# Kernel optimization log

Hardware: AMD Instinct MI355X
Metric: run time of the kernel (lower is better)

The kernel has to match this reference:

```python
import jax, jax.numpy as jnp
import numpy as np

B, S, C, H = 64, 512, 256, 128
P = S  # predict_length defaults to seq_length


def _linear_init(k, fan_in, fan_out):
    bound = 1.0 / np.sqrt(fan_in)
    kw, kb = jax.random.split(k)
    w = jax.random.uniform(kw, (fan_in, fan_out), minval=-bound, maxval=bound, dtype=jnp.float32)
    b = jax.random.uniform(kb, (fan_out,), minval=-bound, maxval=bound, dtype=jnp.float32)
    return w, b


def setup_inputs() -> dict:
    key = jax.random.key(0)
    ks = jax.random.split(key, 10)
    x = jax.random.normal(ks[0], (B, S, C), dtype=jnp.float32)
    wq1, bq1 = _linear_init(ks[1], S, H)
    wk1, bk1 = _linear_init(ks[2], S, H)
    wq2, bq2 = _linear_init(ks[3], S // 2, H)
    wk2, bk2 = _linear_init(ks[4], S // 2, H)
    wq3, bq3 = _linear_init(ks[5], S // 4, H)
    wk3, bk3 = _linear_init(ks[6], S // 4, H)
    wv, bv = _linear_init(ks[7], S, S)
    wo, bo = _linear_init(ks[8], S, P)
    return dict(x=x, wq1=wq1, bq1=bq1, wk1=wk1, bk1=bk1,
                wq2=wq2, bq2=bq2, wk2=wk2, bk2=bk2,
                wq3=wq3, bq3=bq3, wk3=wk3, bk3=bk3,
                wv=wv, bv=bv, wo=wo, bo=bo)


def _channel_attn(xl, wq, bq, wk, bk):
    # xl: [b', C, L]; q,k: [b', C, H]; returns softmax channel-attention [b', C, C]
    q = xl @ wq + bq
    k = xl @ wk + bk
    scores = jnp.einsum('bch,bdh->bcd', q, k) / jnp.sqrt(jnp.asarray(H, q.dtype))
    return jax.nn.softmax(scores, axis=-1)


def reference(x, wq1, bq1, wk1, bk1, wq2, bq2, wk2, bk2, wq3, bq3, wk3, bk3, wv, bv, wo, bo):
    b, s, c = x.shape
    x1 = jnp.swapaxes(x, -2, -1)                                   # [B, C, S]
    x2 = jnp.swapaxes(x.reshape(b * 2, s // 2, c), -2, -1)          # [2B, C, S/2]
    x3 = jnp.swapaxes(x.reshape(b * 4, s // 4, c), -2, -1)          # [4B, C, S/4]
    a1 = _channel_attn(x1, wq1, bq1, wk1, bk1)                      # [B, C, C]
    a2 = _channel_attn(x2, wq2, bq2, wk2, bk2).reshape(b, 2, c, c).mean(axis=1)
    a3 = _channel_attn(x3, wq3, bq3, wk3, bk3).reshape(b, 4, c, c).mean(axis=1)
    stacked = jnp.stack([a1, a2, a3], axis=0)                       # [3, B, C, C]
    gate = jax.nn.softmax(stacked, axis=0)                          # softmax over scales
    attn = (stacked * gate).sum(axis=0)                             # gated multi-scale combine [B, C, C]
    v = x1 @ wv + bv                                                # [B, C, S]
    out = (attn @ v) @ wo + bo                                      # [B, C, P]
    return jnp.swapaxes(out, -2, -1)                                # [B, P, C]
```

## Files before the change

### kernel.cpp

```cpp
#include <hip/hip_runtime.h>
#include <hip/hip_bf16.h>


typedef __attribute__((ext_vector_type(8))) short bf16x8;
typedef __attribute__((ext_vector_type(4))) float f32x4;
typedef __attribute__((ext_vector_type(8))) unsigned short ushort8;

typedef __attribute__((address_space(1))) void* as1vp;
typedef __attribute__((address_space(3))) void* as3vp;

__device__ __forceinline__ void gl2lds16(const void* g, void* l) {
  __builtin_amdgcn_global_load_lds((as1vp)(void*)g, (as3vp)l, 16, 0, 0);
}

__device__ __forceinline__ float bf2f(unsigned short u) {
  union { unsigned int i; float f; } v; v.i = ((unsigned int)u) << 16; return v.f;
}
__device__ __forceinline__ unsigned short f2bf(float f) {
  union { float f; unsigned int i; } v; v.f = f;
  unsigned int r = v.i + 0x7FFFu + ((v.i >> 16) & 1u);
  return (unsigned short)(r >> 16);
}
__device__ __forceinline__ unsigned long long pack4bf(float a, float b, float c, float d) {
  return (unsigned long long)f2bf(a) | ((unsigned long long)f2bf(b) << 16) |
         ((unsigned long long)f2bf(c) << 32) | ((unsigned long long)f2bf(d) << 48);
}

__global__ void __launch_bounds__(256) tcast_all(
    const float* __restrict__ x,
    const float* __restrict__ wq1, const float* __restrict__ wk1,
    const float* __restrict__ wq2, const float* __restrict__ wk2,
    const float* __restrict__ wq3, const float* __restrict__ wk3,
    const float* __restrict__ wv, const float* __restrict__ wo,
    unsigned short* __restrict__ XT,
    unsigned short* __restrict__ W1, unsigned short* __restrict__ W2,
    unsigned short* __restrict__ W3, unsigned short* __restrict__ WVNT,
    unsigned short* __restrict__ WOT) {
  const int bid = blockIdx.x;
  const int t = threadIdx.x;
  if (bid >= 2168) {
    long i0 = (long)(bid - 2168) * 2048 + t * 8;
    f32x4 a = *(const f32x4*)(wv + i0);
    f32x4 b = *(const f32x4*)(wv + i0 + 4);
    ushort8 o;
#pragma unroll
    for (int j = 0; j < 4; ++j) { o[j] = f2bf(a[j]); o[4 + j] = f2bf(b[j]); }
    *(ushort8*)(WVNT + i0) = o;
    return;
  }
  __shared__ float lds[64][68];
  const float* S; unsigned short* D; int R, Cc, r0, c0, rowoff = 0;
  if (bid < 2048) {
    int bz = bid >> 5, i = bid & 31;
    S = x + (long)bz * 131072; D = XT + (long)bz * 131072;
    R = 512; Cc = 256; r0 = (i & 7) * 64; c0 = (i >> 3) * 64;
  } else {
    int wb = bid - 2048;
    if (wb < 32) {
      int m = wb >> 4, i = wb & 15;
      S = m ? wk1 : wq1; D = W1; R = 512; Cc = 128;
      r0 = (i & 7) * 64; c0 = (i >> 3) * 64; rowoff = m * 128;
    } else if (wb < 48) {
      int m = (wb - 32) >> 3, i = (wb - 32) & 7;
      S = m ? wk2 : wq2; D = W2; R = 256; Cc = 128;
      r0 = (i & 3) * 64; c0 = (i >> 2) * 64; rowoff = m * 128;
    } else if (wb < 56) {
      int m = (wb - 48) >> 2, i = (wb - 48) & 3;
      S = m ? wk3 : wq3; D = W3; R = 128; Cc = 128;
      r0 = (i & 1) * 64; c0 = (i >> 1) * 64; rowoff = m * 128;
    } else {
      int i = wb - 56; S = wo; D = WOT; R = 512; Cc = 512;
      r0 = (i & 7) * 64; c0 = (i >> 3) * 64;
    }
  }
  {
    const int row = t >> 2, cq = (t & 3) * 16;
    const float* Sp = S + (long)(r0 + row) * Cc + c0 + cq;
#pragma unroll
    for (int j = 0; j < 4; ++j)
      *(f32x4*)&lds[row][cq + j * 4] = *(const f32x4*)(Sp + j * 4);
  }
  __syncthreads();
  {
    const int rq = (t & 15) * 4, ccb = t >> 4;
#pragma unroll
    for (int j = 0; j < 4; ++j) {
      int cc = ccb + j * 16;
      *(unsigned long long*)(D + (long)(c0 + cc + rowoff) * R + r0 + rq) =
          pack4bf(lds[rq][cc], lds[rq + 1][cc], lds[rq + 2][cc], lds[rq + 3][cc]);
    }
  }
}

__global__ void __launch_bounds__(512) proj_all8(
    const unsigned short* __restrict__ XT,
    const unsigned short* __restrict__ W1, const unsigned short* __restrict__ W2,
    const unsigned short* __restrict__ W3,
    const unsigned short* __restrict__ WOT, const unsigned short* __restrict__ WVNT,
    unsigned short* __restrict__ WVOT, float* __restrict__ BVO,
    const float* __restrict__ bv,
    unsigned short* __restrict__ Q1, unsigned short* __restrict__ Q2,
    unsigned short* __restrict__ Q3,
    const float* __restrict__ bq1, const float* __restrict__ bk1,
    const float* __restrict__ bq2, const float* __restrict__ bk2,
    const float* __restrict__ bq3, const float* __restrict__ bk3) {
  extern __shared__ char smem[];
  const int z = blockIdx.z;
  const int t = threadIdx.x, lane = t & 63, wid = t >> 6;

  if (z >= 464) {
    int p0 = (z - 464) * 128 + wid * 16;
    f32x4 b0 = *(const f32x4*)(bv + lane * 8);
    f32x4 b1 = *(const f32x4*)(bv + lane * 8 + 4);
#pragma unroll
    for (int i = 0; i < 16; ++i) {
      int p = p0 + i;
      bf16x8 wrow = *(const bf16x8*)(WOT + (long)p * 512 + lane * 8);
      float s = 0.0f;
#pragma unroll
      for (int j = 0; j < 4; ++j) {
        s += b0[j] * bf2f((unsigned short)wrow[j]);
        s += b1[j] * bf2f((unsigned short)wrow[4 + j]);
      }
#pragma unroll
      for (int off = 1; off < 64; off <<= 1) s += __shfl_xor(s, off, 64);
      if (lane == 0) BVO[p] = s;
    }
    return;
  }

  const int srow = t >> 3, ssl = t & 7;

  if (z >= 448) {
    const int w = z - 448;
    const int m0 = (w >> 2) * 128, n0 = (w & 3) * 128;
    const unsigned short* Ab = WOT + (long)m0 * 512;
    const unsigned short* Bb = WVNT + (long)n0 * 512;
    const int wmb = (wid >> 2) * 64, wnb = (wid & 3) * 32;
    f32x4 acc[4][2] = {};
    auto stageS = [&](int buf, int k0) {
      char* s = smem + buf * 32768;
#pragma unroll
      for (int i = 0; i < 2; ++i) {
        int row = i * 64 + srow;
        gl2lds16(Ab + (long)row * 512 + k0 + (ssl ^ (row & 7)) * 8, s + i * 8192 + t * 16);
        gl2lds16(Bb + (long)row * 512 + k0 + (ssl ^ (row & 7)) * 8, s + 16384 + i * 8192 + t * 16);
      }
    };
    stageS(0, 0);
    stageS(1, 64);
    for (int j = 0; j < 8; ++j) {
      if (j < 7) asm volatile("s_waitcnt vmcnt(4)" ::: "memory");
      else       asm volatile("s_waitcnt vmcnt(0)" ::: "memory");
      __builtin_amdgcn_s_barrier();
      if (j + 2 < 8) stageS((j + 2) % 3, (j + 2) * 64);
      const char* s = smem + (j % 3) * 32768;
#pragma unroll
      for (int kk = 0; kk < 2; ++kk) {
        const int slot = kk * 4 + (lane >> 4);
        bf16x8 af[4], bfr[2];
#pragma unroll
        for (int mi = 0; mi < 4; ++mi) {
          int row = wmb + mi * 16 + (lane & 15);
          af[mi] = *(const bf16x8*)(s + row * 128 + 16 * (slot ^ (row & 7)));
        }
#pragma unroll
        for (int ni = 0; ni < 2; ++ni) {
          int row = wnb + ni * 16 + (lane & 15);
          bfr[ni] = *(const bf16x8*)(s + 16384 + row * 128 + 16 * (slot ^ (row & 7)));
        }
#pragma unroll
        for (int mi = 0; mi < 4; ++mi)
#pragma unroll
          for (int ni = 0; ni < 2; ++ni)
            acc[mi][ni] = __builtin_amdgcn_mfma_f32_16x16x32_bf16(af[mi], bfr[ni], acc[mi][ni], 0, 0, 0);
      }
    }
#pragma unroll
    for (int ni = 0; ni < 2; ++ni) {
      int col = n0 + wnb + ni * 16 + (lane & 15);
#pragma unroll
      for (int mi = 0; mi < 4; ++mi) {
        int rowb = m0 + wmb + mi * 16 + (lane >> 4) * 4;
#pragma unroll
        for (int r = 0; r < 4; ++r)
          WVOT[(long)(rowb + r) * 512 + col] = f2bf(acc[mi][ni][r]);
      }
    }
    return;
  }

  const unsigned short* Ab; const unsigned short* Bw; unsigned short* O;
  const float *bq, *bk; int K;
  if (z < 64) {
    K = 512; Bw = W1; O = Q1 + (long)z * 65536; bq = bq1; bk = bk1;
    Ab = XT + (long)z * 131072;
  } else if (z < 192) {
    int u = z - 64; K = 256; Bw = W2; O = Q2 + (long)u * 65536; bq = bq2; bk = bk2;
    Ab = XT + (long)(u >> 1) * 131072 + (u & 1) * 256;
  } else {
    int u = z - 192; K = 128; Bw = W3; O = Q3 + (long)u * 65536; bq = bq3; bk = bk3;
    Ab = XT + (long)(u >> 2) * 131072 + (u & 3) * 128;
  }
  const int wmb = (wid >> 1) * 64, wnb = (wid & 1) * 128;

  auto stage = [&](int buf, int k0) {
    char* s = smem + buf * 65536;
#pragma unroll
    for (int i = 0; i < 4; ++i) {
      int row = i * 64 + srow;
      int sc = (ssl ^ (row & 7)) * 8;
      gl2lds16(Ab + (long)row * 512 + k0 + sc, s + i * 8192 + t * 16);
      gl2lds16(Bw + (long)row * K + k0 + sc, s + 32768 + i * 8192 + t * 16);
    }
  };

  f32x4 acc[4][8] = {};
  const int nst = K >> 6;
  stage(0, 0);
  __syncthreads();
  int cur = 0;
  for (int j = 0; j < nst; ++j) {
    if (j + 1 < nst) stage(cur ^ 1, (j + 1) * 64);
    const char* s = smem + cur * 65536;
#pragma unroll
    for (int kk = 0; kk < 2; ++kk) {
      const int slot = kk * 4 + (lane >> 4);
      bf16x8 af[4], bfr[8];
#pragma unroll
      for (int mi = 0; mi < 4; ++mi) {
        int row = wmb + mi * 16 + (lane & 15);
        af[mi] = *(const bf16x8*)(s + row * 128 + 16 * (slot ^ (row & 7)));
      }
#pragma unroll
      for (int ni = 0; ni < 8; ++ni) {
        int row = wnb + ni * 16 + (lane & 15);
        bfr[ni] = *(const bf16x8*)(s + 32768 + row * 128 + 16 * (slot ^ (row & 7)));
      }
#pragma unroll
      for (int mi = 0; mi < 4; ++mi)
#pragma unroll
        for (int ni = 0; ni < 8; ++ni)
          acc[mi][ni] = __builtin_amdgcn_mfma_f32_16x16x32_bf16(af[mi], bfr[ni], acc[mi][ni], 0, 0, 0);
    }
    __syncthreads();
    cur ^= 1;
  }
#pragma unroll
  for (int ni = 0; ni < 8; ++ni) {
    int colL = wnb + ni * 16 + (lane & 15);
    float bv_ = (colL < 128) ? bq[colL] : bk[colL - 128];
#pragma unroll
    for (int mi = 0; mi < 4; ++mi) {
      int rowb = wmb + mi * 16 + (lane >> 4) * 4;
#pragma unroll
      for (int r = 0; r < 4; ++r)
        O[(long)(rowb + r) * 256 + colL] = f2bf(acc[mi][ni][r] + bv_);
    }
  }
}

__global__ void __launch_bounds__(256) scores_mean(
    const unsigned short* __restrict__ QK2, const unsigned short* __restrict__ QK3,
    unsigned short* __restrict__ A2P, unsigned short* __restrict__ A3P) {
  __shared__ unsigned short Qs[64 * 64];
  __shared__ unsigned short Ks[256 * 64];
  const int bid = blockIdx.x;
  const unsigned short* QK; unsigned short* Aout; int NS, b, m0idx;
  if (bid < 256) { NS = 4; b = bid >> 2; m0idx = bid & 3; QK = QK3; Aout = A3P; }
  else { int u = bid - 256; NS = 2; b = u >> 2; m0idx = u & 3; QK = QK2; Aout = A2P; }
  const int m0 = m0idx * 64;
  const int t = threadIdx.x, lane = t & 63, w = t >> 6;
  const int r8 = t >> 3, sl = t & 7;
  const float sc = 0.088388347648318447f;
  const float invNS = 1.0f / NS;
  f32x4 avg[16] = {};
  for (int h = 0; h < NS; ++h) {
    const unsigned short* base = QK + ((long)(b * NS + h) << 16);
    f32x4 acc[16] = {};
    for (int kc = 0; kc < 2; ++kc) {
#pragma unroll
      for (int i = 0; i < 2; ++i) {
        int row = i * 32 + r8;
        gl2lds16(base + (long)(m0 + row) * 256 + kc * 64 + (sl ^ (row & 7)) * 8,
                 (char*)Qs + i * 4096 + t * 16);
      }
#pragma unroll
      for (int i = 0; i < 8; ++i) {
        int row = i * 32 + r8;
        gl2lds16(base + (long)row * 256 + 128 + kc * 64 + (sl ^ (row & 7)) * 8,
                 (char*)Ks + i * 4096 + t * 16);
      }
      __syncthreads();
#pragma unroll
      for (int kk = 0; kk < 2; ++kk) {
        const int qrow = w * 16 + (lane & 15);
        const int slot = kk * 4 + (lane >> 4);
        bf16x8 qf = *(const bf16x8*)((char*)Qs + qrow * 128 + 16 * (slot ^ (qrow & 7)));
#pragma unroll
        for (int ni = 0; ni < 16; ++ni) {
          int krow = ni * 16 + (lane & 15);
          bf16x8 kf = *(const bf16x8*)((char*)Ks + krow * 128 + 16 * (slot ^ (krow & 7)));
          acc[ni] = __builtin_amdgcn_mfma_f32_16x16x32_bf16(qf, kf, acc[ni], 0, 0, 0);
        }
      }
      __syncthreads();
    }
#pragma unroll
    for (int r = 0; r < 4; ++r) {
      float mx = -1e30f;
#pragma unroll
      for (int ni = 0; ni < 16; ++ni) mx = fmaxf(mx, acc[ni][r]);
#pragma unroll
      for (int off = 1; off < 16; off <<= 1) mx = fmaxf(mx, __shfl_xor(mx, off, 64));
      float s = 0.0f;
#pragma unroll
      for (int ni = 0; ni < 16; ++ni) {
        float p = __expf((acc[ni][r] - mx) * sc);
        acc[ni][r] = p;
        s += p;
      }
#pragma unroll
      for (int off = 1; off < 16; off <<= 1) s += __shfl_xor(s, off, 64);
      float f = invNS / s;
#pragma unroll
      for (int ni = 0; ni < 16; ++ni) avg[ni][r] += acc[ni][r] * f;
    }
  }
  unsigned short* Of = Aout + (((long)b * 4 + m0idx) * 256 + t) * 64;
#pragma unroll
  for (int r = 0; r < 4; ++r) {
    ushort8 lo, hi;
#pragma unroll
    for (int j = 0; j < 8; ++j) { lo[j] = f2bf(avg[j][r]); hi[j] = f2bf(avg[8 + j][r]); }
    *(ushort8*)(Of + r * 16) = lo;
    *(ushort8*)(Of + r * 16 + 8) = hi;
  }
}

__global__ void __launch_bounds__(256) scores1_gate(
    const unsigned short* __restrict__ QK1, const unsigned short* __restrict__ A2P,
    const unsigned short* __restrict__ A3P, unsigned short* __restrict__ ATTN) {
  __shared__ unsigned short Qs[64 * 64];
  __shared__ unsigned short Ks[256 * 64];
  const int bid = blockIdx.x;
  const int b = bid >> 2, m0 = (bid & 3) * 64;
  const unsigned short* base = QK1 + ((long)b << 16);
  const int t = threadIdx.x, lane = t & 63, w = t >> 6;
  const int r8 = t >> 3, sl = t & 7;
  f32x4 acc[16] = {};
  for (int kc = 0; kc < 2; ++kc) {
#pragma unroll
    for (int i = 0; i < 2; ++i) {
      int row = i * 32 + r8;
      gl2lds16(base + (long)(m0 + row) * 256 + kc * 64 + (sl ^ (row & 7)) * 8,
               (char*)Qs + i * 4096 + t * 16);
    }
#pragma unroll
    for (int i = 0; i < 8; ++i) {
      int row = i * 32 + r8;
      gl2lds16(base + (long)row * 256 + 128 + kc * 64 + (sl ^ (row & 7)) * 8,
               (char*)Ks + i * 4096 + t * 16);
    }
    __syncthreads();
#pragma unroll
    for (int kk = 0; kk < 2; ++kk) {
      const int qrow = w * 16 + (lane & 15);
      const int slot = kk * 4 + (lane >> 4);
      bf16x8 qf = *(const bf16x8*)((char*)Qs + qrow * 128 + 16 * (slot ^ (qrow & 7)));
#pragma unroll
      for (int ni = 0; ni < 16; ++ni) {
        int krow = ni * 16 + (lane & 15);
        bf16x8 kf = *(const bf16x8*)((char*)Ks + krow * 128 + 16 * (slot ^ (krow & 7)));
        acc[ni] = __builtin_amdgcn_mfma_f32_16x16x32_bf16(qf, kf, acc[ni], 0, 0, 0);
      }
    }
    __syncthreads();
  }
  const float sc = 0.088388347648318447f;
#pragma unroll
  for (int r = 0; r < 4; ++r) {
    float mx = -1e30f;
#pragma unroll
    for (int ni = 0; ni < 16; ++ni) mx = fmaxf(mx, acc[ni][r]);
#pragma unroll
    for (int off = 1; off < 16; off <<= 1) mx = fmaxf(mx, __shfl_xor(mx, off, 64));
    float s = 0.0f;
#pragma unroll
    for (int ni = 0; ni < 16; ++ni) {
      float p = __expf((acc[ni][r] - mx) * sc);
      acc[ni][r] = p;
      s += p;
    }
#pragma unroll
    for (int off = 1; off < 16; off <<= 1) s += __shfl_xor(s, off, 64);
    float inv = 1.0f / s;
    long fidx = ((long)bid * 256 + t) * 64 + r * 16;
    ushort8 a2l = *(const ushort8*)(A2P + fidx);
    ushort8 a2h = *(const ushort8*)(A2P + fidx + 8);
    ushort8 a3l = *(const ushort8*)(A3P + fidx);
    ushort8 a3h = *(const ushort8*)(A3P + fidx + 8);
    int row = m0 + w * 16 + (lane >> 4) * 4 + r;
    long roff = ((long)b << 16) + (long)row * 256 + (lane & 15);
#pragma unroll
    for (int j = 0; j < 8; ++j) {
      float A1 = acc[j][r] * inv;
      float A2 = bf2f(a2l[j]), A3 = bf2f(a3l[j]);
      float m = fmaxf(A1, fmaxf(A2, A3));
      float e1 = __expf(A1 - m), e2 = __expf(A2 - m), e3 = __expf(A3 - m);
      ATTN[roff + j * 16] = f2bf((A1 * e1 + A2 * e2 + A3 * e3) / (e1 + e2 + e3));
    }
#pragma unroll
    for (int j = 0; j < 8; ++j) {
      float A1 = acc[8 + j][r] * inv;
      float A2 = bf2f(a2h[j]), A3 = bf2f(a3h[j]);
      float m = fmaxf(A1, fmaxf(A2, A3));
      float e1 = __expf(A1 - m), e2 = __expf(A2 - m), e3 = __expf(A3 - m);
      ATTN[roff + (8 + j) * 16] = f2bf((A1 * e1 + A2 * e2 + A3 * e3) / (e1 + e2 + e3));
    }
  }
}

template <int F32OUT, int BIASMODE>
__global__ void __launch_bounds__(512) gemm8(
    const unsigned short* __restrict__ A, const unsigned short* __restrict__ B,
    void* __restrict__ OutV, const float* __restrict__ bias,
    int lda, int ldb, int K, long astr, long bstr, long ostr, int ldo) {
  extern __shared__ char smem[];
  const int t = threadIdx.x, lane = t & 63, wid = t >> 6;
  const int wmb = (wid >> 1) * 64, wnb = (wid & 1) * 64;
  const int m0 = blockIdx.y * 256, n0 = blockIdx.x * 128;
  const int bz = blockIdx.z;
  const unsigned short* Ab = A + (long)bz * astr + (long)m0 * lda;
  const unsigned short* Bb = B + (long)bz * bstr + (long)n0 * ldb;
  const int srow = t >> 3, ssl = t & 7;

  auto stage = [&](int buf, int k0) {
    char* s = smem + buf * 49152;
#pragma unroll
    for (int i = 0; i < 4; ++i) {
      int row = i * 64 + srow;
      gl2lds16(Ab + (long)row * lda + k0 + (ssl ^ (row & 7)) * 8, s + i * 8192 + t * 16);
    }
#pragma unroll
    for (int i = 0; i < 2; ++i) {
      int row = i * 64 + srow;
      gl2lds16(Bb + (long)row * ldb + k0 + (ssl ^ (row & 7)) * 8,
               s + 32768 + i * 8192 + t * 16);
    }
  };

  f32x4 acc[4][4] = {};
  const int nst = K >> 6;
  stage(0, 0);
  stage(1, 64);
  for (int j = 0; j < nst; ++j) {
    if (j + 1 < nst) asm volatile("s_waitcnt vmcnt(6)" ::: "memory");
    else             asm volatile("s_waitcnt vmcnt(0)" ::: "memory");
    __builtin_amdgcn_s_barrier();
    if (j + 2 < nst) stage((j + 2) % 3, (j + 2) * 64);
    const char* s = smem + (j % 3) * 49152;
#pragma unroll
    for (int kk = 0; kk < 2; ++kk) {
      const int slot = kk * 4 + (lane >> 4);
      bf16x8 af[4], bfr[4];
#pragma unroll
      for (int mi = 0; mi < 4; ++mi) {
        int row = wmb + mi * 16 + (lane & 15);
        af[mi] = *(const bf16x8*)(s + row * 128 + 16 * (slot ^ (row & 7)));
      }
#pragma unroll
      for (int ni = 0; ni < 4; ++ni) {
        int row = wnb + ni * 16 + (lane & 15);
        bfr[ni] = *(const bf16x8*)(s + 32768 + row * 128 + 16 * (slot ^ (row & 7)));
      }
#pragma unroll
      for (int mi = 0; mi < 4; ++mi)
#pragma unroll
        for (int ni = 0; ni < 4; ++ni)
          acc[mi][ni] = __builtin_amdgcn_mfma_f32_16x16x32_bf16(af[mi], bfr[ni], acc[mi][ni], 0, 0, 0);
    }
  }
#pragma unroll
  for (int mi = 0; mi < 4; ++mi) {
    int rowb = m0 + wmb + mi * 16 + (lane >> 4) * 4;
    float rb[4];
#pragma unroll
    for (int r = 0; r < 4; ++r) rb[r] = (BIASMODE == 2) ? bias[rowb + r] : 0.0f;
#pragma unroll
    for (int ni = 0; ni < 4; ++ni) {
      int col = n0 + wnb + ni * 16 + (lane & 15);
#pragma unroll
      for (int r = 0; r < 4; ++r) {
        float v = acc[mi][ni][r] + rb[r];
        if constexpr (F32OUT)
          ((float*)OutV)[(long)bz * ostr + (long)(rowb + r) * ldo + col] = v;
        else
          ((unsigned short*)OutV)[(long)bz * ostr + (long)(rowb + r) * ldo + col] = f2bf(v);
      }
    }
  }
}

extern "C" void kernel_launch(void* const* d_in, const int* in_sizes, int n_in,
                              void* d_out, int out_size, void* d_ws, size_t ws_size,
                              hipStream_t stream) {
  (void)in_sizes; (void)n_in; (void)out_size; (void)ws_size;
  const float* x   = (const float*)d_in[0];
  const float* wq1 = (const float*)d_in[1];
  const float* bq1 = (const float*)d_in[2];
  const float* wk1 = (const float*)d_in[3];
  const float* bk1 = (const float*)d_in[4];
  const float* wq2 = (const float*)d_in[5];
  const float* bq2 = (const float*)d_in[6];
  const float* wk2 = (const float*)d_in[7];
  const float* bk2 = (const float*)d_in[8];
  const float* wq3 = (const float*)d_in[9];
  const float* bq3 = (const float*)d_in[10];
  const float* wk3 = (const float*)d_in[11];
  const float* bk3 = (const float*)d_in[12];
  const float* wv  = (const float*)d_in[13];
  const float* bv  = (const float*)d_in[14];
  const float* wo  = (const float*)d_in[15];
  const float* bo  = (const float*)d_in[16];
  char* ws = (char*)d_ws;

  unsigned short* XT   = (unsigned short*)(ws + 0);
  unsigned short* WQK1 = (unsigned short*)(ws + 16777216);
  unsigned short* WQK2 = (unsigned short*)(ws + 17039360);
  unsigned short* WQK3 = (unsigned short*)(ws + 17170432);
  unsigned short* WOT  = (unsigned short*)(ws + 17235968);
  unsigned short* WVNT = (unsigned short*)(ws + 17760256);
  unsigned short* WVOT = (unsigned short*)(ws + 18284544);
  float*          BVO  = (float*)(ws + 18808832);
  unsigned short* QK1  = (unsigned short*)(ws + 18876416);
  unsigned short* QK2  = (unsigned short*)(ws + 27265024);
  unsigned short* QK3  = (unsigned short*)(ws + 44042240);
  unsigned short* A2P  = (unsigned short*)(ws + 77596672);
  unsigned short* A3P  = (unsigned short*)(ws + 85985280);
  unsigned short* ATTN = (unsigned short*)(ws + 44042240);
  unsigned short* XVT  = (unsigned short*)(ws + 18876416);

  tcast_all<<<dim3(2296), dim3(256), 0, stream>>>(
      x, wq1, wk1, wq2, wk2, wq3, wk3, wv, wo,
      XT, WQK1, WQK2, WQK3, WVNT, WOT);

  proj_all8<<<dim3(1, 1, 468), dim3(512), 131072, stream>>>(
      XT, WQK1, WQK2, WQK3, WOT, WVNT, WVOT, BVO, bv,
      QK1, QK2, QK3, bq1, bk1, bq2, bk2, bq3, bk3);

  scores_mean<<<dim3(512), dim3(256), 0, stream>>>(QK2, QK3, A2P, A3P);
  scores1_gate<<<dim3(256), dim3(256), 0, stream>>>(QK1, A2P, A3P, ATTN);

  gemm8<0, 2><<<dim3(2, 2, 64), dim3(512), 147456, stream>>>(
      WVOT, XT, XVT, BVO, 512, 512, 512, 0, 131072, 131072, 256);
  gemm8<1, 2><<<dim3(2, 2, 64), dim3(512), 147456, stream>>>(
      XVT, ATTN, d_out, bo, 256, 256, 256, 131072, 65536, 131072, 256);
}
```

Baseline: 114.7 us.

## Fuse channel-attention scores and softmax into projection kernel, gate in separate pass

The projection kernel now keeps each block's Q/K tile in shared memory (transposed via swapped MFMA operands), computes the full 256x256 channel scores and the row softmax in place, and writes per-sub-batch attention fragments. This removes the global round trip of the Q/K projections and replaces two score kernels with one gate kernel that averages the scale fragments and applies the cross-scale softmax. The cost is more global traffic for un-averaged A2/A3 fragments, extra registers and work per projection block, and a longer tail for that kernel.

Result: slower. 153.5 us (+33.8%).

```diff
diff --git a/kernel.cpp b/kernel.cpp
--- a/kernel.cpp
+++ b/kernel.cpp
@@ -92,15 +92,15 @@
   }
 }
 
-__global__ void __launch_bounds__(512) proj_all8(
+__global__ void __launch_bounds__(512) projscore(
     const unsigned short* __restrict__ XT,
     const unsigned short* __restrict__ W1, const unsigned short* __restrict__ W2,
     const unsigned short* __restrict__ W3,
     const unsigned short* __restrict__ WOT, const unsigned short* __restrict__ WVNT,
     unsigned short* __restrict__ WVOT, float* __restrict__ BVO,
     const float* __restrict__ bv,
-    unsigned short* __restrict__ Q1, unsigned short* __restrict__ Q2,
-    unsigned short* __restrict__ Q3,
+    unsigned short* __restrict__ A1F, unsigned short* __restrict__ A2F,
+    unsigned short* __restrict__ A3F,
     const float* __restrict__ bq1, const float* __restrict__ bk1,
     const float* __restrict__ bq2, const float* __restrict__ bk2,
     const float* __restrict__ bq3, const float* __restrict__ bk3) {
@@ -190,16 +190,16 @@
     return;
   }
 
-  const unsigned short* Ab; const unsigned short* Bw; unsigned short* O;
-  const float *bq, *bk; int K;
+  const unsigned short* Ab; const unsigned short* Bw; unsigned short* AF;
+  const float *bq, *bk; int K; long sb;
   if (z < 64) {
-    K = 512; Bw = W1; O = Q1 + (long)z * 65536; bq = bq1; bk = bk1;
+    K = 512; Bw = W1; AF = A1F; sb = z; bq = bq1; bk = bk1;
     Ab = XT + (long)z * 131072;
   } else if (z < 192) {
-    int u = z - 64; K = 256; Bw = W2; O = Q2 + (long)u * 65536; bq = bq2; bk = bk2;
+    int u = z - 64; K = 256; Bw = W2; AF = A2F; sb = u; bq = bq2; bk = bk2;
     Ab = XT + (long)(u >> 1) * 131072 + (u & 1) * 256;
   } else {
-    int u = z - 192; K = 128; Bw = W3; O = Q3 + (long)u * 65536; bq = bq3; bk = bk3;
+    int u = z - 192; K = 128; Bw = W3; AF = A3F; sb = u; bq = bq3; bk = bk3;
     Ab = XT + (long)(u >> 2) * 131072 + (u & 3) * 128;
   }
   const int wmb = (wid >> 1) * 64, wnb = (wid & 1) * 128;
@@ -241,182 +241,134 @@
       for (int mi = 0; mi < 4; ++mi)
 #pragma unroll
         for (int ni = 0; ni < 8; ++ni)
-          acc[mi][ni] = __builtin_amdgcn_mfma_f32_16x16x32_bf16(af[mi], bfr[ni], acc[mi][ni], 0, 0, 0);
+          acc[mi][ni] = __builtin_amdgcn_mfma_f32_16x16x32_bf16(bfr[ni], af[mi], acc[mi][ni], 0, 0, 0);
     }
     __syncthreads();
     cur ^= 1;
   }
-#pragma unroll
-  for (int ni = 0; ni < 8; ++ni) {
-    int colL = wnb + ni * 16 + (lane & 15);
-    float bv_ = (colL < 128) ? bq[colL] : bk[colL - 128];
+
+  {
+    const int chB = (wid & 1) ? 65536 : 0;
+    const float* bias = (wid & 1) ? bk : bq;
 #pragma unroll
     for (int mi = 0; mi < 4; ++mi) {
-      int rowb = wmb + mi * 16 + (lane >> 4) * 4;
-#pragma unroll
-      for (int r = 0; r < 4; ++r)
-        O[(long)(rowb + r) * 256 + colL] = f2bf(acc[mi][ni][r] + bv_);
-    }
-  }
-}
-
-__global__ void __launch_bounds__(256) scores_mean(
-    const unsigned short* __restrict__ QK2, const unsigned short* __restrict__ QK3,
-    unsigned short* __restrict__ A2P, unsigned short* __restrict__ A3P) {
-  __shared__ unsigned short Qs[64 * 64];
-  __shared__ unsigned short Ks[256 * 64];
-  const int bid = blockIdx.x;
-  const unsigned short* QK; unsigned short* Aout; int NS, b, m0idx;
-  if (bid < 256) { NS = 4; b = bid >> 2; m0idx = bid & 3; QK = QK3; Aout = A3P; }
-  else { int u = bid - 256; NS = 2; b = u >> 2; m0idx = u & 3; QK = QK2; Aout = A2P; }
-  const int m0 = m0idx * 64;
-  const int t = threadIdx.x, lane = t & 63, w = t >> 6;
-  const int r8 = t >> 3, sl = t & 7;
+      int rowm = wmb + mi * 16 + (lane & 15);
+#pragma unroll
+      for (int ni = 0; ni < 8; ++ni) {
+        int h = ni * 16 + (lane >> 4) * 4;
+        int addr = chB + (h >> 6) * 32768 + rowm * 128 +
+                   16 * ((((h & 63) >> 3)) ^ (rowm & 7)) + (h & 7) * 2;
+        *(unsigned long long*)(smem + addr) =
+            pack4bf(acc[mi][ni][0] + bias[h], acc[mi][ni][1] + bias[h + 1],
+                    acc[mi][ni][2] + bias[h + 2], acc[mi][ni][3] + bias[h + 3]);
+      }
+    }
+  }
+  __syncthreads();
+
+  f32x4 acc2[2][16] = {};
+#pragma unroll
+  for (int kc = 0; kc < 2; ++kc)
+#pragma unroll
+    for (int kk = 0; kk < 2; ++kk) {
+      const int slot = kk * 4 + (lane >> 4);
+      bf16x8 qf[2];
+#pragma unroll
+      for (int m2 = 0; m2 < 2; ++m2) {
+        int qrow = wid * 32 + m2 * 16 + (lane & 15);
+        qf[m2] = *(const bf16x8*)(smem + kc * 32768 + qrow * 128 + 16 * (slot ^ (qrow & 7)));
+      }
+#pragma unroll
+      for (int ni = 0; ni < 16; ++ni) {
+        int krow = ni * 16 + (lane & 15);
+        bf16x8 kf = *(const bf16x8*)(smem + 65536 + kc * 32768 + krow * 128 + 16 * (slot ^ (krow & 7)));
+        acc2[0][ni] = __builtin_amdgcn_mfma_f32_16x16x32_bf16(qf[0], kf, acc2[0][ni], 0, 0, 0);
+        acc2[1][ni] = __builtin_amdgcn_mfma_f32_16x16x32_bf16(qf[1], kf, acc2[1][ni], 0, 0, 0);
+      }
+    }
+
   const float sc = 0.088388347648318447f;
-  const float invNS = 1.0f / NS;
-  f32x4 avg[16] = {};
-  for (int h = 0; h < NS; ++h) {
-    const unsigned short* base = QK + ((long)(b * NS + h) << 16);
-    f32x4 acc[16] = {};
-    for (int kc = 0; kc < 2; ++kc) {
-#pragma unroll
-      for (int i = 0; i < 2; ++i) {
-        int row = i * 32 + r8;
-        gl2lds16(base + (long)(m0 + row) * 256 + kc * 64 + (sl ^ (row & 7)) * 8,
-                 (char*)Qs + i * 4096 + t * 16);
-      }
-#pragma unroll
-      for (int i = 0; i < 8; ++i) {
-        int row = i * 32 + r8;
-        gl2lds16(base + (long)row * 256 + 128 + kc * 64 + (sl ^ (row & 7)) * 8,
-                 (char*)Ks + i * 4096 + t * 16);
-      }
-      __syncthreads();
-#pragma unroll
-      for (int kk = 0; kk < 2; ++kk) {
-        const int qrow = w * 16 + (lane & 15);
-        const int slot = kk * 4 + (lane >> 4);
-        bf16x8 qf = *(const bf16x8*)((char*)Qs + qrow * 128 + 16 * (slot ^ (qrow & 7)));
-#pragma unroll
-        for (int ni = 0; ni < 16; ++ni) {
-          int krow = ni * 16 + (lane & 15);
-          bf16x8 kf = *(const bf16x8*)((char*)Ks + krow * 128 + 16 * (slot ^ (krow & 7)));
-          acc[ni] = __builtin_amdgcn_mfma_f32_16x16x32_bf16(qf, kf, acc[ni], 0, 0, 0);
-        }
-      }
-      __syncthreads();
-    }
+#pragma unroll
+  for (int m2 = 0; m2 < 2; ++m2) {
+    int quad = (2 * wid + m2) & 3;
+    int m0idx = (2 * wid + m2) >> 2;
+    unsigned short* Of = AF + ((sb * 4 + m0idx) * 256 + quad * 64 + lane) * 64;
 #pragma unroll
     for (int r = 0; r < 4; ++r) {
       float mx = -1e30f;
 #pragma unroll
-      for (int ni = 0; ni < 16; ++ni) mx = fmaxf(mx, acc[ni][r]);
+      for (int ni = 0; ni < 16; ++ni) mx = fmaxf(mx, acc2[m2][ni][r]);
 #pragma unroll
       for (int off = 1; off < 16; off <<= 1) mx = fmaxf(mx, __shfl_xor(mx, off, 64));
       float s = 0.0f;
 #pragma unroll
       for (int ni = 0; ni < 16; ++ni) {
-        float p = __expf((acc[ni][r] - mx) * sc);
-        acc[ni][r] = p;
+        float p = __expf((acc2[m2][ni][r] - mx) * sc);
+        acc2[m2][ni][r] = p;
         s += p;
       }
 #pragma unroll
       for (int off = 1; off < 16; off <<= 1) s += __shfl_xor(s, off, 64);
-      float f = invNS / s;
-#pragma unroll
-      for (int ni = 0; ni < 16; ++ni) avg[ni][r] += acc[ni][r] * f;
-    }
-  }
-  unsigned short* Of = Aout + (((long)b * 4 + m0idx) * 256 + t) * 64;
+      float inv = 1.0f / s;
+      ushort8 lo, hi;
+#pragma unroll
+      for (int j = 0; j < 8; ++j) {
+        lo[j] = f2bf(acc2[m2][j][r] * inv);
+        hi[j] = f2bf(acc2[m2][8 + j][r] * inv);
+      }
+      *(ushort8*)(Of + r * 16) = lo;
+      *(ushort8*)(Of + r * 16 + 8) = hi;
+    }
+  }
+}
+
+__global__ void __launch_bounds__(256) gate_frag(
+    const unsigned short* __restrict__ A1F, const unsigned short* __restrict__ A2F,
+    const unsigned short* __restrict__ A3F, unsigned short* __restrict__ ATTN) {
+  const int bid = blockIdx.x;
+  const int b = bid >> 2, mt = bid & 3;
+  const int t = threadIdx.x, lane = t & 63;
+  const long i1 = (((long)b * 4 + mt) * 256 + t) * 64;
+  const long i2 = (((long)b * 8 + mt) * 256 + t) * 64;
+  const long i3 = (((long)b * 16 + mt) * 256 + t) * 64;
+  const long SBS = 65536;
+  int row = mt * 64 + (t >> 6) * 16 + ((lane >> 4)) * 4;
+  long roffb = ((long)b << 16) + (long)row * 256 + (lane & 15);
 #pragma unroll
   for (int r = 0; r < 4; ++r) {
-    ushort8 lo, hi;
-#pragma unroll
-    for (int j = 0; j < 8; ++j) { lo[j] = f2bf(avg[j][r]); hi[j] = f2bf(avg[8 + j][r]); }
-    *(ushort8*)(Of + r * 16) = lo;
-    *(ushort8*)(Of + r * 16 + 8) = hi;
-  }
-}
-
-__global__ void __launch_bounds__(256) scores1_gate(
-    const unsigned short* __restrict__ QK1, const unsigned short* __restrict__ A2P,
-    const unsigned short* __restrict__ A3P, unsigned short* __restrict__ ATTN) {
-  __shared__ unsigned short Qs[64 * 64];
-  __shared__ unsigned short Ks[256 * 64];
-  const int bid = blockIdx.x;
-  const int b = bid >> 2, m0 = (bid & 3) * 64;
-  const unsigned short* base = QK1 + ((long)b << 16);
-  const int t = threadIdx.x, lane = t & 63, w = t >> 6;
-  const int r8 = t >> 3, sl = t & 7;
-  f32x4 acc[16] = {};
-  for (int kc = 0; kc < 2; ++kc) {
-#pragma unroll
-    for (int i = 0; i < 2; ++i) {
-      int row = i * 32 + r8;
-      gl2lds16(base + (long)(m0 + row) * 256 + kc * 64 + (sl ^ (row & 7)) * 8,
-               (char*)Qs + i * 4096 + t * 16);
-    }
-#pragma unroll
-    for (int i = 0; i < 8; ++i) {
-      int row = i * 32 + r8;
-      gl2lds16(base + (long)row * 256 + 128 + kc * 64 + (sl ^ (row & 7)) * 8,
-               (char*)Ks + i * 4096 + t * 16);
-    }
-    __syncthreads();
-#pragma unroll
-    for (int kk = 0; kk < 2; ++kk) {
-      const int qrow = w * 16 + (lane & 15);
-      const int slot = kk * 4 + (lane >> 4);
-      bf16x8 qf = *(const bf16x8*)((char*)Qs + qrow * 128 + 16 * (slot ^ (qrow & 7)));
-#pragma unroll
-      for (int ni = 0; ni < 16; ++ni) {
-        int krow = ni * 16 + (lane & 15);
-        bf16x8 kf = *(const bf16x8*)((char*)Ks + krow * 128 + 16 * (slot ^ (krow & 7)));
-        acc[ni] = __builtin_amdgcn_mfma_f32_16x16x32_bf16(qf, kf, acc[ni], 0, 0, 0);
-      }
-    }
-    __syncthreads();
-  }
-  const float sc = 0.088388347648318447f;
-#pragma unroll
-  for (int r = 0; r < 4; ++r) {
-    float mx = -1e30f;
-#pragma unroll
-    for (int ni = 0; ni < 16; ++ni) mx = fmaxf(mx, acc[ni][r]);
-#pragma unroll
-    for (int off = 1; off < 16; off <<= 1) mx = fmaxf(mx, __shfl_xor(mx, off, 64));
-    float s = 0.0f;
-#pragma unroll
-    for (int ni = 0; ni < 16; ++ni) {
-      float p = __expf((acc[ni][r] - mx) * sc);
-      acc[ni][r] = p;
-      s += p;
-    }
-#pragma unroll
-    for (int off = 1; off < 16; off <<= 1) s += __shfl_xor(s, off, 64);
-    float inv = 1.0f / s;
-    long fidx = ((long)bid * 256 + t) * 64 + r * 16;
-    ushort8 a2l = *(const ushort8*)(A2P + fidx);
-    ushort8 a2h = *(const ushort8*)(A2P + fidx + 8);
-    ushort8 a3l = *(const ushort8*)(A3P + fidx);
-    ushort8 a3h = *(const ushort8*)(A3P + fidx + 8);
-    int row = m0 + w * 16 + (lane >> 4) * 4 + r;
-    long roff = ((long)b << 16) + (long)row * 256 + (lane & 15);
+    int f = r * 16;
+    ushort8 a1l = *(const ushort8*)(A1F + i1 + f);
+    ushort8 a1h = *(const ushort8*)(A1F + i1 + f + 8);
+    ushort8 a2l0 = *(const ushort8*)(A2F + i2 + f);
+    ushort8 a2h0 = *(const ushort8*)(A2F + i2 + f + 8);
+    ushort8 a2l1 = *(const ushort8*)(A2F + i2 + SBS + f);
+    ushort8 a2h1 = *(const ushort8*)(A2F + i2 + SBS + f + 8);
+    ushort8 a3l0 = *(const ushort8*)(A3F + i3 + f);
+    ushort8 a3h0 = *(const ushort8*)(A3F + i3 + f + 8);
+    ushort8 a3l1 = *(const ushort8*)(A3F + i3 + SBS + f);
+    ushort8 a3h1 = *(const ushort8*)(A3F + i3 + SBS + f + 8);
+    ushort8 a3l2 = *(const ushort8*)(A3F + i3 + 2 * SBS + f);
+    ushort8 a3h2 = *(const ushort8*)(A3F + i3 + 2 * SBS + f + 8);
+    ushort8 a3l3 = *(const ushort8*)(A3F + i3 + 3 * SBS + f);
+    ushort8 a3h3 = *(const ushort8*)(A3F + i3 + 3 * SBS + f + 8);
+    long ro = roffb + (long)r * 256;
 #pragma unroll
     for (int j = 0; j < 8; ++j) {
-      float A1 = acc[j][r] * inv;
-      float A2 = bf2f(a2l[j]), A3 = bf2f(a3l[j]);
+      float A1 = bf2f(a1l[j]);
+      float A2 = 0.5f * (bf2f(a2l0[j]) + bf2f(a2l1[j]));
+      float A3 = 0.25f * (bf2f(a3l0[j]) + bf2f(a3l1[j]) + bf2f(a3l2[j]) + bf2f(a3l3[j]));
       float m = fmaxf(A1, fmaxf(A2, A3));
       float e1 = __expf(A1 - m), e2 = __expf(A2 - m), e3 = __expf(A3 - m);
-      ATTN[roff + j * 16] = f2bf((A1 * e1 + A2 * e2 + A3 * e3) / (e1 + e2 + e3));
+      ATTN[ro + j * 16] = f2bf((A1 * e1 + A2 * e2 + A3 * e3) / (e1 + e2 + e3));
     }
 #pragma unroll
     for (int j = 0; j < 8; ++j) {
-      float A1 = acc[8 + j][r] * inv;
-      float A2 = bf2f(a2h[j]), A3 = bf2f(a3h[j]);
+      float A1 = bf2f(a1h[j]);
+      float A2 = 0.5f * (bf2f(a2h0[j]) + bf2f(a2h1[j]));
+      float A3 = 0.25f * (bf2f(a3h0[j]) + bf2f(a3h1[j]) + bf2f(a3h2[j]) + bf2f(a3h3[j]));
       float m = fmaxf(A1, fmaxf(A2, A3));
       float e1 = __expf(A1 - m), e2 = __expf(A2 - m), e3 = __expf(A3 - m);
-      ATTN[roff + (8 + j) * 16] = f2bf((A1 * e1 + A2 * e2 + A3 * e3) / (e1 + e2 + e3));
+      ATTN[ro + (8 + j) * 16] = f2bf((A1 * e1 + A2 * e2 + A3 * e3) / (e1 + e2 + e3));
     }
   }
 }
@@ -533,24 +485,21 @@
   unsigned short* WVNT = (unsigned short*)(ws + 17760256);
   unsigned short* WVOT = (unsigned short*)(ws + 18284544);
   float*          BVO  = (float*)(ws + 18808832);
-  unsigned short* QK1  = (unsigned short*)(ws + 18876416);
-  unsigned short* QK2  = (unsigned short*)(ws + 27265024);
-  unsigned short* QK3  = (unsigned short*)(ws + 44042240);
-  unsigned short* A2P  = (unsigned short*)(ws + 77596672);
-  unsigned short* A3P  = (unsigned short*)(ws + 85985280);
-  unsigned short* ATTN = (unsigned short*)(ws + 44042240);
+  unsigned short* A1F  = (unsigned short*)(ws + 18876416);
+  unsigned short* A2F  = (unsigned short*)(ws + 27265024);
+  unsigned short* A3F  = (unsigned short*)(ws + 44042240);
+  unsigned short* ATTN = (unsigned short*)(ws + 77596672);
   unsigned short* XVT  = (unsigned short*)(ws + 18876416);
 
   tcast_all<<<dim3(2296), dim3(256), 0, stream>>>(
       x, wq1, wk1, wq2, wk2, wq3, wk3, wv, wo,
       XT, WQK1, WQK2, WQK3, WVNT, WOT);
 
-  proj_all8<<<dim3(1, 1, 468), dim3(512), 131072, stream>>>(
+  projscore<<<dim3(1, 1, 468), dim3(512), 131072, stream>>>(
       XT, WQK1, WQK2, WQK3, WOT, WVNT, WVOT, BVO, bv,
-      QK1, QK2, QK3, bq1, bk1, bq2, bk2, bq3, bk3);
-
-  scores_mean<<<dim3(512), dim3(256), 0, stream>>>(QK2, QK3, A2P, A3P);
-  scores1_gate<<<dim3(256), dim3(256), 0, stream>>>(QK1, A2P, A3P, ATTN);
+      A1F, A2F, A3F, bq1, bk1, bq2, bk2, bq3, bk3);
+
+  gate_frag<<<dim3(256), dim3(256), 0, stream>>>(A1F, A2F, A3F, ATTN);
 
   gemm8<0, 2><<<dim3(2, 2, 64), dim3(512), 147456, stream>>>(
       WVOT, XT, XVT, BVO, 512, 512, 512, 0, 131072, 131072, 256);
```
